# Optimization experiments

Measured on AMD Instinct MI355X. Metric: run time of the kernel, lower is better.

## Reference

```python
import jax, jax.numpy as jnp
import numpy as np

HEADS = 4
HEAD_DIM = 128  # GATConv out_channels
NEG_SLOPE_ATT = 0.2   # GATConv internal leaky relu
NEG_SLOPE_ACT = 0.01  # nn.LeakyReLU() default


def gat_conv(x, edge_index, W, att_src, att_dst, bias):
    # x: [N, F]; edge_index: [2, E] (row 0 = src j, row 1 = dst i)
    N = x.shape[0]
    h = (x @ W).reshape(N, HEADS, HEAD_DIM)            # [N, H, C]
    loops = jnp.arange(N, dtype=edge_index.dtype)
    src = jnp.concatenate([edge_index[0], loops])      # add self loops
    dst = jnp.concatenate([edge_index[1], loops])
    a_src = jnp.einsum('nhc,hc->nh', h, att_src)       # [N, H]
    a_dst = jnp.einsum('nhc,hc->nh', h, att_dst)
    e = jax.nn.leaky_relu(a_src[src] + a_dst[dst], NEG_SLOPE_ATT)  # [E', H]
    # segment softmax over incoming edges of each dst node
    emax = jax.ops.segment_max(e, dst, num_segments=N)
    ex = jnp.exp(e - emax[dst])
    denom = jax.ops.segment_sum(ex, dst, num_segments=N)
    alpha = ex / (denom[dst] + 1e-16)                  # [E', H]
    msg = h[src] * alpha[:, :, None]                   # [E', H, C]
    out = jax.ops.segment_sum(msg, dst, num_segments=N)
    return out.reshape(N, HEADS * HEAD_DIM) + bias     # [N, H*C]


def branch(x, edge_index, W, att_src, att_dst, bias, fc1_w, fc1_b):
    h = gat_conv(x, edge_index, W, att_src, att_dst, bias)
    h = jax.nn.leaky_relu(h, NEG_SLOPE_ACT)
    g = jnp.mean(h, axis=0, keepdims=True)             # global mean pool, batch all zeros -> [1, H*C]
    g = jax.nn.leaky_relu(g @ fc1_w + fc1_b, NEG_SLOPE_ACT)
    return g  # dropout is identity in eval mode


def setup_inputs() -> dict:
    key = jax.random.key(0)
    ks = jax.random.split(key, 10)
    N, E, F = 20000, 320000, 512
    HC = HEADS * HEAD_DIM
    s = 1.0 / np.sqrt(F)
    return {
        'x': jax.random.normal(ks[0], (N, F), jnp.float32),
        'adj': jax.random.randint(ks[1], (2, E), 0, N, jnp.int64),
        'wt_x': jax.random.normal(ks[2], (N, F), jnp.float32),
        'wt_adj': jax.random.randint(ks[3], (2, E), 0, N, jnp.int64),
        'W': jax.random.normal(ks[4], (F, HC), jnp.float32) * s,
        'att_src': jax.random.normal(ks[5], (HEADS, HEAD_DIM), jnp.float32) * s,
        'att_dst': jax.random.normal(ks[6], (HEADS, HEAD_DIM), jnp.float32) * s,
        'bias': jnp.zeros((HC,), jnp.float32),
        'fc1_w': jax.random.normal(ks[7], (HC, 512), jnp.float32) * (1.0 / np.sqrt(HC)),
        'fc1_b': jnp.zeros((512,), jnp.float32),
    }


def reference(x, adj, wt_x, wt_adj, W, att_src, att_dst, bias, fc1_w, fc1_b):
    g = branch(x, adj, W, att_src, att_dst, bias, fc1_w, fc1_b)
    wt_g = branch(wt_x, wt_adj, W, att_src, att_dst, bias, fc1_w, fc1_b)
    xd = g - wt_g
    return jnp.concatenate([g, wt_g, xd], axis=1)  # [1, 3*512]
```

## Files before the change

kernel.cpp:

```cpp
#include <hip/hip_runtime.h>
#include <hip/hip_bf16.h>

typedef unsigned short u16;
typedef short bf16x8 __attribute__((ext_vector_type(8)));
typedef float f32x4 __attribute__((ext_vector_type(4)));
typedef float f32x2 __attribute__((ext_vector_type(2)));

__device__ __forceinline__ u16 f2b(float f) {
    unsigned x = __float_as_uint(f);
    return (u16)((x + 0x7fffu + ((x >> 16) & 1u)) >> 16);
}

__device__ __forceinline__ int pkbf(float lo, float hi) {
    return __builtin_amdgcn_perm(__float_as_uint(hi), __float_as_uint(lo), 0x07060302);
}

__global__ void cast_wt_kernel(const float* __restrict__ W, u16* __restrict__ Wt) {
    int idx = blockIdx.x * blockDim.x + threadIdx.x;
    int n = idx >> 9, k = idx & 511;
    Wt[idx] = f2b(W[k * 512 + n]);
}

__global__ __launch_bounds__(256, 2) void gemm_fused2(
    const float* __restrict__ xA, const float* __restrict__ xW, const u16* __restrict__ Bt,
    unsigned char* __restrict__ h8, const float* __restrict__ att_src,
    const float* __restrict__ att_dst, float* __restrict__ asrc, float* __restrict__ adst,
    int N, int Mpad) {
    __shared__ float lA[128 * 32];
    __shared__ u16 lB[128 * 32];
    __shared__ float sred[2][128][2];
    const int tid = threadIdx.x;
    const int w = tid >> 6, l = tid & 63;
    const int row0 = blockIdx.y * 128;
    const int head = blockIdx.x;
    const int col0 = head * 128;
    const int wr = w >> 1, wc = w & 1;
    const int mlane = l & 15, quad = l >> 4;

    const float* src = (row0 >= Mpad) ? xW : xA;
    const int rbase = row0 - (row0 >= Mpad ? Mpad : 0);
    const int arow = (w << 3) + (l >> 3);
    const int acol = (l & 7) << 2;
    const int srow = (w << 4) + (l >> 2);
    const int scol = (l & 3) << 3;

    f32x4 acc[4][4];
#pragma unroll
    for (int i = 0; i < 4; i++)
#pragma unroll
        for (int j = 0; j < 4; j++) acc[i][j] = f32x4{0.f, 0.f, 0.f, 0.f};

    for (int k0 = 0; k0 < 512; k0 += 32) {
#pragma unroll
        for (int g = 0; g < 4; ++g) {
            int lrow = rbase + g * 32 + arow;
            lrow = min(lrow, N - 1);
            const float* ga = src + (size_t)lrow * 512 + k0 + acol;
            float* la = lA + (g * 32 + (w << 3)) * 32;
            __builtin_amdgcn_global_load_lds((const __attribute__((address_space(1))) void*)ga,
                                             (__attribute__((address_space(3))) void*)la, 16, 0, 0);
        }
#pragma unroll
        for (int s = 0; s < 2; ++s) {
            const u16* gb = Bt + (size_t)(col0 + s * 64 + srow) * 512 + (k0 + scol);
            u16* lb = lB + s * 2048 + w * 512;
            __builtin_amdgcn_global_load_lds((const __attribute__((address_space(1))) void*)gb,
                                             (__attribute__((address_space(3))) void*)lb, 16, 0, 0);
        }
        __syncthreads();
        bf16x8 af[4], bfr[4];
#pragma unroll
        for (int i = 0; i < 4; i++) {
            const float* ap = &lA[(wr * 64 + i * 16 + mlane) * 32 + quad * 8];
            float4 f0 = *(const float4*)ap;
            float4 f1 = *(const float4*)(ap + 4);
            int* ai = (int*)&af[i];
            ai[0] = pkbf(f0.x, f0.y);
            ai[1] = pkbf(f0.z, f0.w);
            ai[2] = pkbf(f1.x, f1.y);
            ai[3] = pkbf(f1.z, f1.w);
            bfr[i] = *(const bf16x8*)&lB[(wc * 64 + i * 16 + mlane) * 32 + quad * 8];
        }
#pragma unroll
        for (int i = 0; i < 4; i++)
#pragma unroll
            for (int j = 0; j < 4; j++)
                acc[i][j] = __builtin_amdgcn_mfma_f32_16x16x32_bf16(af[i], bfr[j], acc[i][j], 0, 0, 0);
        __syncthreads();
    }

    float as_j[4], ad_j[4];
#pragma unroll
    for (int j = 0; j < 4; j++) {
        as_j[j] = att_src[col0 + wc * 64 + j * 16 + mlane];
        ad_j[j] = att_dst[col0 + wc * 64 + j * 16 + mlane];
    }
#pragma unroll
    for (int i = 0; i < 4; i++) {
#pragma unroll
        for (int r = 0; r < 4; r++) {
            float vs = 0.f, vd = 0.f;
#pragma unroll
            for (int j = 0; j < 4; j++) {
                float hv = acc[i][j][r];
                vs += hv * as_j[j];
                vd += hv * ad_j[j];
            }
#pragma unroll
            for (int o = 8; o >= 1; o >>= 1) {
                vs += __shfl_xor(vs, o);
                vd += __shfl_xor(vd, o);
            }
            if (mlane == 0) {
                int lrow = wr * 64 + i * 16 + quad * 4 + r;
                sred[0][lrow][wc] = vs;
                sred[1][lrow][wc] = vd;
            }
        }
    }
#pragma unroll
    for (int i = 0; i < 4; i++)
#pragma unroll
        for (int j = 0; j < 4; j++)
#pragma unroll
            for (int r = 0; r < 4; r++) {
                int rg = row0 + wr * 64 + i * 16 + quad * 4 + r;
                int cg = col0 + wc * 64 + j * 16 + mlane;
                float v = acc[i][j][r];
                unsigned pk = __builtin_amdgcn_cvt_pk_fp8_f32(v, v, 0, false);
                h8[(size_t)rg * 512 + cg] = (unsigned char)(pk & 0xff);
            }
    __syncthreads();
    {
        int row = tid & 127, which = tid >> 7;
        int rg = row0 + row;
        float v = sred[which][row][0] + sred[which][row][1];
        (which ? adst : asrc)[(rg << 2) + head] = v;
    }
}

__global__ void csr_count(const int* __restrict__ adj, const int* __restrict__ wadj,
                          int E, int Mpad, int* __restrict__ deg) {
    int i = blockIdx.x * blockDim.x + threadIdx.x;
    if (i < 2 * E) {
        int d = (i < E) ? adj[E + i] : (wadj[E + (i - E)] + Mpad);
        atomicAdd(&deg[d], 1);
    }
}

__global__ __launch_bounds__(256) void scanA(const int* __restrict__ deg, int* __restrict__ off,
                                             int* __restrict__ bsum, int n, int N, int Mpad) {
    __shared__ int wsum[4];
    int tid = threadIdx.x, lane = tid & 63, wid = tid >> 6;
    int i = blockIdx.x * 256 + tid;
    int valid = (i < N) || (i >= Mpad && i < Mpad + N);
    int d = (i < n) ? deg[i] + (valid ? 1 : 0) : 0;
    int x = d;
#pragma unroll
    for (int o = 1; o < 64; o <<= 1) {
        int y = __shfl_up(x, (unsigned)o, 64);
        if (lane >= o) x += y;
    }
    if (lane == 63) wsum[wid] = x;
    __syncthreads();
    int woff = 0;
    for (int j = 0; j < wid; ++j) woff += wsum[j];
    if (i < n) off[i] = woff + x - d;
    if (tid == 255) bsum[blockIdx.x] = woff + x;
}

__global__ __launch_bounds__(256) void scanB(const int* __restrict__ bsum, int* __restrict__ bbase,
                                             int nb, int* __restrict__ off, int n) {
    __shared__ int wsum[4];
    int tid = threadIdx.x, lane = tid & 63, wid = tid >> 6;
    int d = (tid < nb) ? bsum[tid] : 0;
    int x = d;
#pragma unroll
    for (int o = 1; o < 64; o <<= 1) {
        int y = __shfl_up(x, (unsigned)o, 64);
        if (lane >= o) x += y;
    }
    if (lane == 63) wsum[wid] = x;
    __syncthreads();
    int woff = 0;
    for (int j = 0; j < wid; ++j) woff += wsum[j];
    int excl = woff + x - d;
    if (tid < nb) bbase[tid] = excl;
    if (tid == nb - 1) off[n] = excl + d;
}

__global__ void scanC(int* __restrict__ off, const int* __restrict__ bbase,
                      int* __restrict__ cursor, int* __restrict__ csrc, int n, int N, int Mpad) {
    int i = blockIdx.x * blockDim.x + threadIdx.x;
    if (i < n) {
        int o = off[i] + bbase[i >> 8];
        off[i] = o;
        int valid = (i < N) || (i >= Mpad && i < Mpad + N);
        if (valid) csrc[o] = i;
        cursor[i] = o + valid;
    }
}

__global__ void csr_scatter(const int* __restrict__ adj, const int* __restrict__ wadj,
                            int E, int Mpad, int* __restrict__ cursor, int* __restrict__ csrc) {
    int i = blockIdx.x * blockDim.x + threadIdx.x;
    if (i < 2 * E) {
        int s, d;
        if (i < E) {
            s = adj[i];
            d = adj[E + i];
        } else {
            s = wadj[i - E] + Mpad;
            d = wadj[E + (i - E)] + Mpad;
        }
        int p = atomicAdd(&cursor[d], 1);
        csrc[p] = s;
    }
}

__device__ __forceinline__ void edge2(int hr, float ad, int head, const float* __restrict__ asrc,
                                      const unsigned char* __restrict__ h8, int c,
                                      float* acc, float& dsum) {
    float e = asrc[(hr << 2) + head] + ad;
    e = fmaxf(e, 0.2f * e);
    float ex = __expf(e);
    dsum += ex;
    int2 hv = *(const int2*)(h8 + (((size_t)hr) << 9) + c);
    f32x2 f01 = __builtin_amdgcn_cvt_pk_f32_fp8(hv.x, false);
    f32x2 f23 = __builtin_amdgcn_cvt_pk_f32_fp8(hv.x, true);
    f32x2 f45 = __builtin_amdgcn_cvt_pk_f32_fp8(hv.y, false);
    f32x2 f67 = __builtin_amdgcn_cvt_pk_f32_fp8(hv.y, true);
    acc[0] += ex * f01.x; acc[1] += ex * f01.y;
    acc[2] += ex * f23.x; acc[3] += ex * f23.y;
    acc[4] += ex * f45.x; acc[5] += ex * f45.y;
    acc[6] += ex * f67.x; acc[7] += ex * f67.y;
}

__global__ __launch_bounds__(256) void gat_aggregate6(
    const unsigned char* __restrict__ h8, const float* __restrict__ asrc,
    const float* __restrict__ adst, const int* __restrict__ off, const int* __restrict__ csrc,
    const float* __restrict__ bias, float* __restrict__ partAB, int Mpad) {
    __shared__ float spool[1024];
    int tid = threadIdx.x;
    for (int i = tid; i < 1024; i += 256) spool[i] = 0.f;
    __syncthreads();
    int wv = tid >> 6, l = tid & 63;
    int c = l << 3;
    int head = l >> 4;
    float bb[8];
#pragma unroll
    for (int k = 0; k < 8; ++k) bb[k] = bias[c + k];
    float poolA[8] = {0.f, 0.f, 0.f, 0.f, 0.f, 0.f, 0.f, 0.f};
    float poolB[8] = {0.f, 0.f, 0.f, 0.f, 0.f, 0.f, 0.f, 0.f};
    const int npairs = Mpad;
    const int stride = gridDim.x << 2;
    for (int pr = (blockIdx.x << 2) + wv; pr < npairs; pr += stride) {
        int d0 = pr << 1, d1 = d0 + 1;
        int q0 = off[d0], q1 = off[d0 + 1], q2 = off[d0 + 2];
        int n0 = q1 - q0, n1 = q2 - q1;
        float ad0 = adst[(d0 << 2) + head];
        float ad1 = adst[(d1 << 2) + head];
        float acc0[8] = {0.f, 0.f, 0.f, 0.f, 0.f, 0.f, 0.f, 0.f};
        float acc1[8] = {0.f, 0.f, 0.f, 0.f, 0.f, 0.f, 0.f, 0.f};
        float dsum0 = 0.f, dsum1 = 0.f;
        int m = n0 < n1 ? n0 : n1;
        int i = 0;
        for (; i + 2 <= m; i += 2) {
            int2 ca = *(const int2*)(csrc + q0 + i);
            int2 cb = *(const int2*)(csrc + q1 + i);
            edge2(ca.x, ad0, head, asrc, h8, c, acc0, dsum0);
            edge2(cb.x, ad1, head, asrc, h8, c, acc1, dsum1);
            edge2(ca.y, ad0, head, asrc, h8, c, acc0, dsum0);
            edge2(cb.y, ad1, head, asrc, h8, c, acc1, dsum1);
        }
        for (int j = i; j < n0; ++j) edge2(csrc[q0 + j], ad0, head, asrc, h8, c, acc0, dsum0);
        for (int j = i; j < n1; ++j) edge2(csrc[q1 + j], ad1, head, asrc, h8, c, acc1, dsum1);
        bool isB = d0 >= Mpad;
        float* pool = isB ? poolB : poolA;
        if (n0 > 0) {
            float inv = 1.f / (dsum0 + 1e-16f);
#pragma unroll
            for (int k = 0; k < 8; ++k) {
                float o = acc0[k] * inv + bb[k];
                pool[k] += fmaxf(o, 0.01f * o);
            }
        }
        if (n1 > 0) {
            float inv = 1.f / (dsum1 + 1e-16f);
#pragma unroll
            for (int k = 0; k < 8; ++k) {
                float o = acc1[k] * inv + bb[k];
                pool[k] += fmaxf(o, 0.01f * o);
            }
        }
    }
#pragma unroll
    for (int k = 0; k < 8; ++k) {
        atomicAdd(&spool[c + k], poolA[k]);
        atomicAdd(&spool[512 + c + k], poolB[k]);
    }
    __syncthreads();
    int base = (blockIdx.x & 63) << 9;
    for (int i = tid; i < 1024; i += 256) {
        float* dp = (i < 512) ? (partAB + base + i) : (partAB + 64 * 512 + base + (i - 512));
        atomicAdd(dp, spool[i]);
    }
}

__global__ __launch_bounds__(256) void fc_final2(
    const float* __restrict__ partAB, const float* __restrict__ w, const float* __restrict__ b,
    float* __restrict__ out, float invN) {
    __shared__ float gA[512], gB[512];
    __shared__ float rA[256], rB[256];
    int t = threadIdx.x;
    for (int i = t; i < 512; i += 256) {
        float sA = 0.f, sB = 0.f;
        for (int r = 0; r < 64; ++r) {
            sA += partAB[r * 512 + i];
            sB += partAB[64 * 512 + r * 512 + i];
        }
        gA[i] = sA * invN;
        gB[i] = sB * invN;
    }
    __syncthreads();
    int jj = t & 31, ks = t >> 5;
    int j = blockIdx.x * 32 + jj;
    float sA = 0.f, sB = 0.f;
    for (int k = ks * 64; k < ks * 64 + 64; ++k) {
        float wv = w[k * 512 + j];
        sA += gA[k] * wv;
        sB += gB[k] * wv;
    }
    rA[t] = sA;
    rB[t] = sB;
    __syncthreads();
    if (ks == 0) {
#pragma unroll
        for (int s2 = 1; s2 < 8; ++s2) {
            sA += rA[jj + 32 * s2];
            sB += rB[jj + 32 * s2];
        }
        sA += b[j];
        sB += b[j];
        sA = sA >= 0.f ? sA : 0.01f * sA;
        sB = sB >= 0.f ? sB : 0.01f * sB;
        out[j] = sA;
        out[512 + j] = sB;
        out[1024 + j] = sA - sB;
    }
}

extern "C" void kernel_launch(void* const* d_in, const int* in_sizes, int n_in,
                              void* d_out, int out_size, void* d_ws, size_t ws_size,
                              hipStream_t stream) {
    const float* x = (const float*)d_in[0];
    const int* adj = (const int*)d_in[1];
    const float* wtx = (const float*)d_in[2];
    const int* wadj = (const int*)d_in[3];
    const float* W = (const float*)d_in[4];
    const float* att_s = (const float*)d_in[5];
    const float* att_d = (const float*)d_in[6];
    const float* bias = (const float*)d_in[7];
    const float* fc1w = (const float*)d_in[8];
    const float* fc1b = (const float*)d_in[9];
    float* out = (float*)d_out;

    const int N = in_sizes[0] / 512;
    const int E = in_sizes[1] / 2;
    const int Mpad = ((N + 127) / 128) * 128;
    const int R2 = 2 * Mpad;
    const int nb = (R2 + 255) / 256;

    char* p = (char*)d_ws;
    auto alloc = [&](size_t bytes) -> char* {
        char* r = p;
        p += (bytes + 255) & ~(size_t)255;
        return r;
    };
    unsigned char* h8 = (unsigned char*)alloc((size_t)R2 * 512);
    u16* Wt = (u16*)alloc(512 * 512 * 2);
    float* asrc = (float*)alloc((size_t)R2 * 4 * 4);
    float* adst = (float*)alloc((size_t)R2 * 4 * 4);
    int* deg = (int*)alloc((size_t)R2 * 4);
    int* off = (int*)alloc((size_t)(R2 + 1) * 4);
    int* cursor = (int*)alloc((size_t)R2 * 4);
    int* bsum = (int*)alloc(256 * 4);
    int* bbase = (int*)alloc(256 * 4);
    int* csrc = (int*)alloc((size_t)2 * (E + N) * 4);
    float* partAB = (float*)alloc((size_t)2 * 64 * 512 * 4);

    hipMemsetAsync(partAB, 0, (size_t)2 * 64 * 512 * 4, stream);
    hipMemsetAsync(deg, 0, (size_t)R2 * 4, stream);
    cast_wt_kernel<<<(512 * 512) / 256, 256, 0, stream>>>(W, Wt);

    csr_count<<<(2 * E + 255) / 256, 256, 0, stream>>>(adj, wadj, E, Mpad, deg);
    scanA<<<nb, 256, 0, stream>>>(deg, off, bsum, R2, N, Mpad);
    scanB<<<1, 256, 0, stream>>>(bsum, bbase, nb, off, R2);
    scanC<<<nb, 256, 0, stream>>>(off, bbase, cursor, csrc, R2, N, Mpad);
    csr_scatter<<<(2 * E + 255) / 256, 256, 0, stream>>>(adj, wadj, E, Mpad, cursor, csrc);

    dim3 gg(4, R2 / 128, 1);
    gemm_fused2<<<gg, 256, 0, stream>>>(x, wtx, Wt, h8, att_s, att_d, asrc, adst, N, Mpad);

    gat_aggregate6<<<2048, 256, 0, stream>>>(h8, asrc, adst, off, csrc, bias, partAB, Mpad);

    fc_final2<<<16, 256, 0, stream>>>(partAB, fc1w, fc1b, out, 1.0f / (float)N);
}
```

Before: 357.6 us.

## Store features head-major and aggregate one head per block

The GEMM epilogue now writes the fp8 features and the attention logits in a head-major layout ([head][row][128]). The aggregation kernel gives each block a single head, chosen from the block index, and has each wave handle four destination nodes at once, one per 16-lane group. The intent is a per-head working set that fits better in cache, since the gathered rows are 128 bytes instead of 512. The cost is divergent edge loops, padded up to the wave's maximum degree with masked dummy edges, and four times as many passes over the destination nodes per head.

Measured after the change: 372.1 us. 1.04x slower.

```diff
diff --git a/kernel.cpp b/kernel.cpp
--- a/kernel.cpp
+++ b/kernel.cpp
@@ -36,6 +36,7 @@
     const int col0 = head * 128;
     const int wr = w >> 1, wc = w & 1;
     const int mlane = l & 15, quad = l >> 4;
+    const int R2v = 2 * Mpad;
 
     const float* src = (row0 >= Mpad) ? xW : xA;
     const int rbase = row0 - (row0 >= Mpad ? Mpad : 0);
@@ -125,17 +126,17 @@
 #pragma unroll
             for (int r = 0; r < 4; r++) {
                 int rg = row0 + wr * 64 + i * 16 + quad * 4 + r;
-                int cg = col0 + wc * 64 + j * 16 + mlane;
+                int cc = wc * 64 + j * 16 + mlane;
                 float v = acc[i][j][r];
                 unsigned pk = __builtin_amdgcn_cvt_pk_fp8_f32(v, v, 0, false);
-                h8[(size_t)rg * 512 + cg] = (unsigned char)(pk & 0xff);
+                h8[(((size_t)(head * R2v + rg)) << 7) + cc] = (unsigned char)(pk & 0xff);
             }
     __syncthreads();
     {
         int row = tid & 127, which = tid >> 7;
         int rg = row0 + row;
         float v = sred[which][row][0] + sred[which][row][1];
-        (which ? adst : asrc)[(rg << 2) + head] = v;
+        (which ? adst : asrc)[head * R2v + rg] = v;
     }
 }
 
@@ -218,14 +219,16 @@
     }
 }
 
-__device__ __forceinline__ void edge2(int hr, float ad, int head, const float* __restrict__ asrc,
-                                      const unsigned char* __restrict__ h8, int c,
+__device__ __forceinline__ void edgeH(int hr, bool valid, float ad,
+                                      const float* __restrict__ ash,
+                                      const unsigned char* __restrict__ h8h, int ch,
                                       float* acc, float& dsum) {
-    float e = asrc[(hr << 2) + head] + ad;
+    float e = ash[hr] + ad;
     e = fmaxf(e, 0.2f * e);
     float ex = __expf(e);
+    ex = valid ? ex : 0.f;
     dsum += ex;
-    int2 hv = *(const int2*)(h8 + (((size_t)hr) << 9) + c);
+    int2 hv = *(const int2*)(h8h + (((size_t)hr) << 7) + ch);
     f32x2 f01 = __builtin_amdgcn_cvt_pk_f32_fp8(hv.x, false);
     f32x2 f23 = __builtin_amdgcn_cvt_pk_f32_fp8(hv.x, true);
     f32x2 f45 = __builtin_amdgcn_cvt_pk_f32_fp8(hv.y, false);
@@ -236,74 +239,86 @@
     acc[6] += ex * f67.x; acc[7] += ex * f67.y;
 }
 
-__global__ __launch_bounds__(256) void gat_aggregate6(
+__global__ __launch_bounds__(256) void gat_aggregate7(
     const unsigned char* __restrict__ h8, const float* __restrict__ asrc,
     const float* __restrict__ adst, const int* __restrict__ off, const int* __restrict__ csrc,
     const float* __restrict__ bias, float* __restrict__ partAB, int Mpad) {
-    __shared__ float spool[1024];
+    const int R2 = 2 * Mpad;
+    __shared__ float spool[256];
     int tid = threadIdx.x;
-    for (int i = tid; i < 1024; i += 256) spool[i] = 0.f;
+    spool[tid] = 0.f;
     __syncthreads();
     int wv = tid >> 6, l = tid & 63;
-    int c = l << 3;
-    int head = l >> 4;
+    int g = l >> 4;
+    int ch = (l & 15) << 3;
+    int head = (blockIdx.x & 7) >> 1;
+    const unsigned char* h8h = h8 + (((size_t)head * R2) << 7);
+    const float* ash = asrc + (size_t)head * R2;
+    const float* adh = adst + (size_t)head * R2;
     float bb[8];
 #pragma unroll
-    for (int k = 0; k < 8; ++k) bb[k] = bias[c + k];
+    for (int k = 0; k < 8; ++k) bb[k] = bias[head * 128 + ch + k];
     float poolA[8] = {0.f, 0.f, 0.f, 0.f, 0.f, 0.f, 0.f, 0.f};
     float poolB[8] = {0.f, 0.f, 0.f, 0.f, 0.f, 0.f, 0.f, 0.f};
-    const int npairs = Mpad;
-    const int stride = gridDim.x << 2;
-    for (int pr = (blockIdx.x << 2) + wv; pr < npairs; pr += stride) {
-        int d0 = pr << 1, d1 = d0 + 1;
-        int q0 = off[d0], q1 = off[d0 + 1], q2 = off[d0 + 2];
-        int n0 = q1 - q0, n1 = q2 - q1;
-        float ad0 = adst[(d0 << 2) + head];
-        float ad1 = adst[(d1 << 2) + head];
-        float acc0[8] = {0.f, 0.f, 0.f, 0.f, 0.f, 0.f, 0.f, 0.f};
-        float acc1[8] = {0.f, 0.f, 0.f, 0.f, 0.f, 0.f, 0.f, 0.f};
-        float dsum0 = 0.f, dsum1 = 0.f;
-        int m = n0 < n1 ? n0 : n1;
+
+    int widx = ((((blockIdx.x >> 3) << 1) | (blockIdx.x & 1)) << 2) + wv;
+    const int nquad = R2 >> 2;
+    for (int q = widx; q < nquad; q += gridDim.x) {
+        int d0 = q << 2;
+        int dg = d0 + g;
+        int qa = off[dg], qb = off[dg + 1];
+        int n = qb - qa;
+        float ad = adh[dg];
+        float acc[8] = {0.f, 0.f, 0.f, 0.f, 0.f, 0.f, 0.f, 0.f};
+        float dsum = 0.f;
+        int nmax = n;
+        nmax = max(nmax, __shfl_xor(nmax, 16));
+        nmax = max(nmax, __shfl_xor(nmax, 32));
         int i = 0;
-        for (; i + 2 <= m; i += 2) {
-            int2 ca = *(const int2*)(csrc + q0 + i);
-            int2 cb = *(const int2*)(csrc + q1 + i);
-            edge2(ca.x, ad0, head, asrc, h8, c, acc0, dsum0);
-            edge2(cb.x, ad1, head, asrc, h8, c, acc1, dsum1);
-            edge2(ca.y, ad0, head, asrc, h8, c, acc0, dsum0);
-            edge2(cb.y, ad1, head, asrc, h8, c, acc1, dsum1);
-        }
-        for (int j = i; j < n0; ++j) edge2(csrc[q0 + j], ad0, head, asrc, h8, c, acc0, dsum0);
-        for (int j = i; j < n1; ++j) edge2(csrc[q1 + j], ad1, head, asrc, h8, c, acc1, dsum1);
-        bool isB = d0 >= Mpad;
-        float* pool = isB ? poolB : poolA;
-        if (n0 > 0) {
-            float inv = 1.f / (dsum0 + 1e-16f);
-#pragma unroll
-            for (int k = 0; k < 8; ++k) {
-                float o = acc0[k] * inv + bb[k];
-                pool[k] += fmaxf(o, 0.01f * o);
+        for (; i + 2 <= nmax; i += 2) {
+            bool v0 = i < n, v1 = i + 1 < n;
+            int i0 = v0 ? qa + i : 0;
+            int i1 = v1 ? qa + i + 1 : 0;
+            int h0 = csrc[i0];
+            int h1 = csrc[i1];
+            edgeH(h0, v0, ad, ash, h8h, ch, acc, dsum);
+            edgeH(h1, v1, ad, ash, h8h, ch, acc, dsum);
+        }
+        if (i < nmax) {
+            bool v0 = i < n;
+            int i0 = v0 ? qa + i : 0;
+            edgeH(csrc[i0], v0, ad, ash, h8h, ch, acc, dsum);
+        }
+        if (n > 0) {
+            float inv = 1.f / (dsum + 1e-16f);
+            if (d0 >= Mpad) {
+#pragma unroll
+                for (int k = 0; k < 8; ++k) {
+                    float o = acc[k] * inv + bb[k];
+                    poolB[k] += fmaxf(o, 0.01f * o);
+                }
+            } else {
+#pragma unroll
+                for (int k = 0; k < 8; ++k) {
+                    float o = acc[k] * inv + bb[k];
+                    poolA[k] += fmaxf(o, 0.01f * o);
+                }
             }
         }
-        if (n1 > 0) {
-            float inv = 1.f / (dsum1 + 1e-16f);
-#pragma unroll
-            for (int k = 0; k < 8; ++k) {
-                float o = acc1[k] * inv + bb[k];
-                pool[k] += fmaxf(o, 0.01f * o);
-            }
-        }
     }
 #pragma unroll
     for (int k = 0; k < 8; ++k) {
-        atomicAdd(&spool[c + k], poolA[k]);
-        atomicAdd(&spool[512 + c + k], poolB[k]);
-    }
-    __syncthreads();
-    int base = (blockIdx.x & 63) << 9;
-    for (int i = tid; i < 1024; i += 256) {
-        float* dp = (i < 512) ? (partAB + base + i) : (partAB + 64 * 512 + base + (i - 512));
-        atomicAdd(dp, spool[i]);
+        atomicAdd(&spool[ch + k], poolA[k]);
+        atomicAdd(&spool[128 + ch + k], poolB[k]);
+    }
+    __syncthreads();
+    {
+        int base = (blockIdx.x & 63) << 9;
+        int c = tid & 127;
+        float v = spool[tid];
+        float* dp = (tid < 128) ? (partAB + base + head * 128 + c)
+                                : (partAB + 64 * 512 + base + head * 128 + c);
+        atomicAdd(dp, v);
     }
 }
 
@@ -402,7 +417,7 @@
     dim3 gg(4, R2 / 128, 1);
     gemm_fused2<<<gg, 256, 0, stream>>>(x, wtx, Wt, h8, att_s, att_d, asrc, adst, N, Mpad);
 
-    gat_aggregate6<<<2048, 256, 0, stream>>>(h8, asrc, adst, off, csrc, bias, partAB, Mpad);
+    gat_aggregate7<<<2048, 256, 0, stream>>>(h8, asrc, adst, off, csrc, bias, partAB, Mpad);
 
     fc_final2<<<16, 256, 0, stream>>>(partAB, fc1w, fc1b, out, 1.0f / (float)N);
 }
```
